# Performance work log

Hardware: AMD Instinct MI355X
Metric: run time of the kernel (lower is better)

The kernel has to match this reference:

```python
import jax, jax.numpy as jnp
import numpy as np

B, T, D, H, O = 256, 256, 256, 1024, 256


def setup_inputs() -> dict:
    key = jax.random.key(0)
    ks = jax.random.split(key, 4)
    x = jax.random.normal(ks[0], (B, T, D), dtype=jnp.float32)
    # Glorot-ish scaling to keep gates/tanh out of saturation
    Wx = jax.random.normal(ks[1], (D + O, 4 * H), dtype=jnp.float32) * 0.05
    Wh = jax.random.normal(ks[2], (H, 4 * H), dtype=jnp.float32) * 0.05
    b = jnp.zeros((4 * H,), dtype=jnp.float32)
    Wd = jax.random.normal(ks[3], (H, O), dtype=jnp.float32) * 0.05
    bd = jnp.zeros((O,), dtype=jnp.float32)
    return {"x": x, "Wx": Wx, "Wh": Wh, "b": b, "Wd": Wd, "bd": bd}


def reference(x, Wx, Wh, b, Wd, bd):
    """Autoregressive LSTM cell unrolled over time with lax.scan.

    Each step: concat(input_t, prev_dense_output) -> LSTMCell (Keras gate
    order i,f,c,o) -> Dense+tanh -> output fed back next step.
    """
    Bz = x.shape[0]
    Hh = Wh.shape[0]
    Oo = Wd.shape[1]
    h0 = jnp.zeros((Bz, Hh), dtype=x.dtype)
    c0 = jnp.zeros((Bz, Hh), dtype=x.dtype)
    y0 = jnp.zeros((Bz, Oo), dtype=x.dtype)  # initial prev_output

    def step(carry, xt):
        h, c, y = carry
        combined = jnp.concatenate([xt, y], axis=-1)  # [B, D+O]
        z = combined @ Wx + h @ Wh + b                # [B, 4H]
        i, f, g, o = jnp.split(z, 4, axis=-1)
        i = jax.nn.sigmoid(i)
        f = jax.nn.sigmoid(f)
        g = jnp.tanh(g)
        o = jax.nn.sigmoid(o)
        c_new = f * c + i * g
        h_new = o * jnp.tanh(c_new)
        y_new = jnp.tanh(h_new @ Wd + bd)             # Dense(tanh)
        return (h_new, c_new, y_new), y_new

    xs = jnp.swapaxes(x, 0, 1)  # [T, B, D]
    _, ys = jax.lax.scan(step, (h0, c0, y0), xs)
    return jnp.swapaxes(ys, 0, 1)  # [B, T, O]
```

## Files before the change

kernel.cpp:

```cpp
#include <hip/hip_runtime.h>


typedef _Float16 f16x8 __attribute__((ext_vector_type(8)));
typedef _Float16 f16x4 __attribute__((ext_vector_type(4)));
typedef float f32x4 __attribute__((ext_vector_type(4)));

#define TSTEPS 256
#define HID 1024
#define OUTD 256
#define KF 1536
#define KA 1280
#define NBLK 256
#define RSLOTS 16
#define SLOTE (256 * KA)

#define RING_OFF   0ull
#define WFULLT_OFF 0ull
#define WDT_OFF    12582912ull
#define XH_OFF     13107200ull
#define CNT_OFF    46661632ull
#define WS_NEEDED  46663680ull

#define HCNT(g) ((g) * 64)
#define YCNT(g) (128 + (g) * 64)

#define LDS_SLAB_BYTES 98304
#define LDS_WDT_BYTES  32768
#define LDS_ZBUF_BYTES 16896
#define LDS_TOTAL (LDS_SLAB_BYTES + LDS_WDT_BYTES + LDS_ZBUF_BYTES)

#define AGENT  __HIP_MEMORY_SCOPE_AGENT

__device__ __forceinline__ float sigf(float x) {
    return 1.0f / (1.0f + __expf(-x));
}
__device__ __forceinline__ float tanhfast(float x) {
    return 1.0f - 2.0f / (__expf(2.0f * x) + 1.0f);
}

__device__ __forceinline__ void garrive(int* base, int j) {
    __syncthreads();
    if (threadIdx.x == 0)
        __hip_atomic_fetch_add(base + j, 1, __ATOMIC_RELAXED, AGENT);
}
__device__ __forceinline__ void gwait(int* base, int target) {
    if (threadIdx.x < 8) {
        while (__hip_atomic_load(base + threadIdx.x, __ATOMIC_RELAXED, AGENT) < target)
            __builtin_amdgcn_s_sleep(2);
    }
    __syncthreads();
}
__device__ __forceinline__ void gwait_both(int* cnts, int target) {
    if (threadIdx.x < 8) {
        while (__hip_atomic_load(cnts + HCNT(0) + threadIdx.x, __ATOMIC_RELAXED, AGENT) < target ||
               __hip_atomic_load(cnts + HCNT(1) + threadIdx.x, __ATOMIC_RELAXED, AGENT) < target)
            __builtin_amdgcn_s_sleep(2);
    }
    __syncthreads();
}

__global__ void prep_w(const float* __restrict__ Wx, const float* __restrict__ Wh,
                       const float* __restrict__ Wd,
                       _Float16* __restrict__ WfullT, _Float16* __restrict__ WdT) {
    int bid = blockIdx.x;
    if (bid < 4096) {
        int n = bid;
        for (int k = threadIdx.x; k < KF; k += 256) {
            float v;
            if (k < 256)       v = Wx[(size_t)k * 4096 + n];
            else if (k < 1280) v = Wh[(size_t)(k - 256) * 4096 + n];
            else               v = Wx[(size_t)(k - 1024) * 4096 + n];
            WfullT[(size_t)n * KF + k] = (_Float16)v;
        }
    } else {
        int o = bid - 4096;
        for (int k = threadIdx.x; k < HID; k += 256) {
            WdT[(size_t)o * HID + k] = (_Float16)Wd[(size_t)k * OUTD + o];
        }
    }
}

__global__ void prep_x(const float* __restrict__ x, _Float16* __restrict__ xh, int* cnts) {
    size_t i0 = ((size_t)blockIdx.x * 256 + threadIdx.x) * 8;
    float4 a = *(const float4*)(x + i0);
    float4 c = *(const float4*)(x + i0 + 4);
    f16x8 v;
    v[0] = (_Float16)a.x; v[1] = (_Float16)a.y; v[2] = (_Float16)a.z; v[3] = (_Float16)a.w;
    v[4] = (_Float16)c.x; v[5] = (_Float16)c.y; v[6] = (_Float16)c.z; v[7] = (_Float16)c.w;
    *(f16x8*)(xh + i0) = v;
    if (blockIdx.x == 0) cnts[threadIdx.x] = 0;
}

template<int NS, typename AL>
__device__ __forceinline__ void gemmPart(AL&& aload, const _Float16* slab, int kbB,
                                         int rl, int kg, f32x4 (&acc)[2][2]) {
    constexpr int PFD = (NS < 12) ? NS : 12;
    f16x8 pa[PFD][2];
#pragma unroll
    for (int i = 0; i < PFD; ++i) { pa[i][0] = aload(i, 0); pa[i][1] = aload(i, 1); }
    const int sw = rl & 7;
    const _Float16* bb0 = slab + (size_t)rl * 1536;
    const _Float16* bb1 = slab + (size_t)(16 + rl) * 1536;
#pragma unroll
    for (int kk = 0; kk < NS; ++kk) {
        int kblk = kbB + kk * 4 + kg;
        int idx = (kblk ^ sw) * 8;
        f16x8 b0 = *(const f16x8*)(bb0 + idx);
        f16x8 b1 = *(const f16x8*)(bb1 + idx);
        f16x8 a0 = pa[kk % PFD][0];
        f16x8 a1 = pa[kk % PFD][1];
        if (kk + PFD < NS) {
            pa[kk % PFD][0] = aload(kk + PFD, 0);
            pa[kk % PFD][1] = aload(kk + PFD, 1);
        }
        acc[0][0] = __builtin_amdgcn_mfma_f32_16x16x32_f16(a0, b0, acc[0][0], 0, 0, 0);
        acc[0][1] = __builtin_amdgcn_mfma_f32_16x16x32_f16(a0, b1, acc[0][1], 0, 0, 0);
        acc[1][0] = __builtin_amdgcn_mfma_f32_16x16x32_f16(a1, b0, acc[1][0], 0, 0, 0);
        acc[1][1] = __builtin_amdgcn_mfma_f32_16x16x32_f16(a1, b1, acc[1][1], 0, 0, 0);
    }
}

__global__ __launch_bounds__(256, 1) void lstm_persist(
        const _Float16* __restrict__ WfullT, const _Float16* __restrict__ WdT,
        const _Float16* __restrict__ xh, const float* __restrict__ b,
        const float* __restrict__ bd,
        _Float16* __restrict__ ring,
        int* cnts, float* __restrict__ out) {
    extern __shared__ char dynsm[];
    _Float16* slab = (_Float16*)dynsm;
    _Float16* wdt  = (_Float16*)(dynsm + LDS_SLAB_BYTES);
    float* zbuf = (float*)(dynsm + LDS_SLAB_BYTES + LDS_WDT_BYTES);

    const int tid = threadIdx.x, bid = blockIdx.x;
    const int w = tid >> 6, lane = tid & 63;
    const int rl = lane & 15, kg = lane >> 4;

    const int bat0 = (bid >> 7) << 7;
    const int n0 = (bid & 127) << 3;
    const int r0 = (bid >> 4) << 4;
    const int c0 = (bid & 15) << 4;
    const int gid = bid >> 7;
    const int subj = (bid >> 4) & 7;

    int* hcnt = cnts + HCNT(gid);
    int* ycnt = cnts + YCNT(gid);

    for (int i = tid; i < 32 * 192; i += 256) {
        int vcol = i / 192, kblk = i % 192;
        int n = (vcol & 3) * 1024 + n0 + (vcol >> 2);
        f16x8 v = *(const f16x8*)(WfullT + (size_t)n * KF + kblk * 8);
        *(f16x8*)(slab + ((size_t)vcol * 192 + (kblk ^ (vcol & 7))) * 8) = v;
    }
    for (int i = tid; i < 16 * 128; i += 256) {
        int wcol = i >> 7, kb = i & 127;
        f16x8 v = *(const f16x8*)(WdT + (size_t)(c0 + wcol) * HID + kb * 8);
        *(f16x8*)(wdt + ((size_t)wcol * 128 + (kb ^ (wcol & 7))) * 8) = v;
    }
    const int trow = tid >> 1;
    const int ccB = (tid & 1) * 4;
    float bb[4][4];
#pragma unroll
    for (int g = 0; g < 4; ++g)
#pragma unroll
        for (int c2 = 0; c2 < 4; ++c2)
            bb[g][c2] = b[g * 1024 + n0 + ccB + c2];
    const float bdv = bd[c0 + (tid & 15)];
    float creg[4] = {0.f, 0.f, 0.f, 0.f};

    const size_t arow = (size_t)(bat0 + w * 32 + rl);

    auto epilogue = [&](f32x4 (&A)[2][2], _Float16* slotW) {
#pragma unroll
        for (int mt = 0; mt < 2; ++mt)
#pragma unroll
            for (int nt = 0; nt < 2; ++nt)
#pragma unroll
                for (int r = 0; r < 4; ++r) {
                    int zrow = w * 32 + mt * 16 + kg * 4 + r;
                    zbuf[zrow * 33 + nt * 16 + rl] = A[mt][nt][r];
                }
        __syncthreads();
        union { f16x4 v; unsigned long long u; } hu;
#pragma unroll
        for (int c2 = 0; c2 < 4; ++c2) {
            int cc = ccB + c2;
            float zi = zbuf[trow * 33 + cc * 4 + 0];
            float zf = zbuf[trow * 33 + cc * 4 + 1];
            float zg = zbuf[trow * 33 + cc * 4 + 2];
            float zo = zbuf[trow * 33 + cc * 4 + 3];
            float iv = sigf(zi + bb[0][c2]);
            float fv = sigf(zf + bb[1][c2]);
            float gv = tanhfast(zg + bb[2][c2]);
            float ov = sigf(zo + bb[3][c2]);
            float cnew = fv * creg[c2] + iv * gv;
            creg[c2] = cnew;
            hu.v[c2] = (_Float16)(ov * tanhfast(cnew));
        }
        __hip_atomic_store(
            (unsigned long long*)(slotW + (size_t)(bat0 + trow) * KA + n0 + ccB),
            hu.u, __ATOMIC_RELAXED, AGENT);
    };

    auto phaseB = [&](int t, _Float16* slotT, const f16x8* wa) {
        const _Float16* hp = slotT + (size_t)(r0 + rl) * KA + (w << 8) + kg * 8;
        f16x8 ha[8];
#pragma unroll
        for (int it = 0; it < 8; ++it)
            ha[it] = *(const f16x8*)(hp + it * 32);
        f32x4 accB; accB[0] = 0.f; accB[1] = 0.f; accB[2] = 0.f; accB[3] = 0.f;
#pragma unroll
        for (int it = 0; it < 8; ++it)
            accB = __builtin_amdgcn_mfma_f32_16x16x32_f16(ha[it], wa[it], accB, 0, 0, 0);
        float* red = zbuf;
#pragma unroll
        for (int r = 0; r < 4; ++r)
            red[w * 256 + (kg * 4 + r) * 16 + rl] = accB[r];
        __syncthreads();
        int rr = tid >> 4, cc = tid & 15;
        float s = red[rr * 16 + cc] + red[256 + rr * 16 + cc] +
                  red[512 + rr * 16 + cc] + red[768 + rr * 16 + cc];
        float y = tanhfast(s + bdv);
        __builtin_nontemporal_store(
            y, out + (size_t)(r0 + rr) * 65536 + (size_t)t * 256 + (c0 + cc));
        union { _Float16 h; unsigned short u; } cv; cv.h = (_Float16)y;
        unsigned short* ys = (unsigned short*)(zbuf + 1024);
        ys[tid] = cv.u;
        __syncthreads();
        if (tid < 64) {
            unsigned long long yv = *(const unsigned long long*)(ys + tid * 4);
            int row = r0 + (tid >> 2), colb = c0 + (tid & 3) * 4;
            __hip_atomic_store(
                (unsigned long long*)(slotT + (size_t)row * KA + 1024 + colb),
                yv, __ATOMIC_RELAXED, AGENT);
        }
    };

    garrive(hcnt, subj);
    gwait_both(cnts, 16);

    f32x4 acc[2][2];
#pragma unroll
    for (int mt = 0; mt < 2; ++mt)
#pragma unroll
        for (int nt = 0; nt < 2; ++nt) {
            acc[mt][nt][0] = 0.f; acc[mt][nt][1] = 0.f;
            acc[mt][nt][2] = 0.f; acc[mt][nt][3] = 0.f;
        }
    {
        const _Float16* xb = xh + arow * 65536 + kg * 8;
        auto loadX = [&](int kk, int mt) -> f16x8 {
            return *(const f16x8*)(xb + (size_t)mt * 16 * 65536 + kk * 32);
        };
        gemmPart<8>(loadX, slab, 0, rl, kg, acc);
    }
    epilogue(acc, ring);
    garrive(hcnt, subj);

    for (int t = 0; t < TSTEPS; ++t) {
        if ((t & 15) == 0)
            __builtin_amdgcn_fence(__ATOMIC_ACQUIRE, "agent");

        _Float16* slotT = ring + (size_t)(t & (RSLOTS - 1)) * SLOTE;

#pragma unroll
        for (int mt = 0; mt < 2; ++mt)
#pragma unroll
            for (int nt = 0; nt < 2; ++nt) {
                acc[mt][nt][0] = 0.f; acc[mt][nt][1] = 0.f;
                acc[mt][nt][2] = 0.f; acc[mt][nt][3] = 0.f;
            }

        if (t < TSTEPS - 1) {
            const _Float16* xb = xh + arow * 65536 + (size_t)(t + 1) * 256 + kg * 8;
            auto loadX = [&](int kk, int mt) -> f16x8 {
                return *(const f16x8*)(xb + (size_t)mt * 16 * 65536 + kk * 32);
            };
            gemmPart<8>(loadX, slab, 0, rl, kg, acc);
        }

        f16x8 wa[8];
#pragma unroll
        for (int it = 0; it < 8; ++it) {
            int kb = (w << 5) + it * 4 + kg;
            wa[it] = *(const f16x8*)(wdt + ((size_t)rl * 128 + (kb ^ (rl & 7))) * 8);
        }

        gwait(hcnt, (t + 2) * 16);
        phaseB(t, slotT, wa);

        if (t < TSTEPS - 1) {
            garrive(ycnt, subj);

            {
                const _Float16* hb = slotT + arow * KA + kg * 8;
                auto loadH = [&](int kk, int mt) -> f16x8 {
                    return *(const f16x8*)(hb + (size_t)mt * 16 * KA + kk * 32);
                };
                gemmPart<32>(loadH, slab, 32, rl, kg, acc);
            }

            gwait(ycnt, (t + 1) * 16);

            {
                const _Float16* yb = slotT + arow * KA + 1024 + kg * 8;
                auto loadY = [&](int kk, int mt) -> f16x8 {
                    return *(const f16x8*)(yb + (size_t)mt * 16 * KA + kk * 32);
                };
                gemmPart<8>(loadY, slab, 160, rl, kg, acc);
            }

            epilogue(acc, ring + (size_t)((t + 1) & (RSLOTS - 1)) * SLOTE);
            garrive(hcnt, subj);
        }
    }
}

extern "C" void kernel_launch(void* const* d_in, const int* in_sizes, int n_in,
                              void* d_out, int out_size, void* d_ws, size_t ws_size,
                              hipStream_t stream) {
    const float* x  = (const float*)d_in[0];
    const float* Wx = (const float*)d_in[1];
    const float* Wh = (const float*)d_in[2];
    const float* b  = (const float*)d_in[3];
    const float* Wd = (const float*)d_in[4];
    const float* bd = (const float*)d_in[5];
    float* out = (float*)d_out;
    char* ws = (char*)d_ws;
    if (ws_size < WS_NEEDED) return;

    _Float16* WfullT = (_Float16*)(ws + WFULLT_OFF);
    _Float16* WdT    = (_Float16*)(ws + WDT_OFF);
    _Float16* xh     = (_Float16*)(ws + XH_OFF);
    _Float16* ring   = (_Float16*)(ws + RING_OFF);
    int*      cnts   = (int*)(ws + CNT_OFF);

    static int lds_set = 0;
    if (!lds_set) {
        hipFuncSetAttribute((const void*)lstm_persist,
                            hipFuncAttributeMaxDynamicSharedMemorySize, LDS_TOTAL);
        lds_set = 1;
    }

    prep_w<<<4352, 256, 0, stream>>>(Wx, Wh, Wd, WfullT, WdT);
    prep_x<<<8192, 256, 0, stream>>>(x, xh, cnts);
    lstm_persist<<<NBLK, 256, LDS_TOTAL, stream>>>(WfullT, WdT, xh, b, bd, ring, cnts, out);
}
```

Before: 4.176 ms.

## Double threads per block and give each wave half the batch rows

The persistent LSTM kernel now launches 512 threads per block, so 8 waves each compute a 16-row M tile instead of 4 waves each doing 32 rows. The aim is more waves in flight to hide global and LDS latency in the serial per-step GEMMs, and fewer live accumulator and prefetch registers per wave. The gate epilogue and the dense-output phase are guarded so only the first 256 threads or first 4 waves do that work. In exchange, every weight fragment in LDS is now read by twice as many waves per step, and block-wide barriers span more waves.

```diff
diff --git a/kernel.cpp b/kernel.cpp
--- a/kernel.cpp
+++ b/kernel.cpp
@@ -93,11 +93,11 @@
 
 template<int NS, typename AL>
 __device__ __forceinline__ void gemmPart(AL&& aload, const _Float16* slab, int kbB,
-                                         int rl, int kg, f32x4 (&acc)[2][2]) {
+                                         int rl, int kg, f32x4 (&acc)[2]) {
     constexpr int PFD = (NS < 12) ? NS : 12;
-    f16x8 pa[PFD][2];
-#pragma unroll
-    for (int i = 0; i < PFD; ++i) { pa[i][0] = aload(i, 0); pa[i][1] = aload(i, 1); }
+    f16x8 pa[PFD];
+#pragma unroll
+    for (int i = 0; i < PFD; ++i) pa[i] = aload(i);
     const int sw = rl & 7;
     const _Float16* bb0 = slab + (size_t)rl * 1536;
     const _Float16* bb1 = slab + (size_t)(16 + rl) * 1536;
@@ -107,20 +107,14 @@
         int idx = (kblk ^ sw) * 8;
         f16x8 b0 = *(const f16x8*)(bb0 + idx);
         f16x8 b1 = *(const f16x8*)(bb1 + idx);
-        f16x8 a0 = pa[kk % PFD][0];
-        f16x8 a1 = pa[kk % PFD][1];
-        if (kk + PFD < NS) {
-            pa[kk % PFD][0] = aload(kk + PFD, 0);
-            pa[kk % PFD][1] = aload(kk + PFD, 1);
-        }
-        acc[0][0] = __builtin_amdgcn_mfma_f32_16x16x32_f16(a0, b0, acc[0][0], 0, 0, 0);
-        acc[0][1] = __builtin_amdgcn_mfma_f32_16x16x32_f16(a0, b1, acc[0][1], 0, 0, 0);
-        acc[1][0] = __builtin_amdgcn_mfma_f32_16x16x32_f16(a1, b0, acc[1][0], 0, 0, 0);
-        acc[1][1] = __builtin_amdgcn_mfma_f32_16x16x32_f16(a1, b1, acc[1][1], 0, 0, 0);
-    }
-}
-
-__global__ __launch_bounds__(256, 1) void lstm_persist(
+        f16x8 a0 = pa[kk % PFD];
+        if (kk + PFD < NS) pa[kk % PFD] = aload(kk + PFD);
+        acc[0] = __builtin_amdgcn_mfma_f32_16x16x32_f16(a0, b0, acc[0], 0, 0, 0);
+        acc[1] = __builtin_amdgcn_mfma_f32_16x16x32_f16(a0, b1, acc[1], 0, 0, 0);
+    }
+}
+
+__global__ __launch_bounds__(512, 2) void lstm_persist(
         const _Float16* __restrict__ WfullT, const _Float16* __restrict__ WdT,
         const _Float16* __restrict__ xh, const float* __restrict__ b,
         const float* __restrict__ bd,
@@ -145,13 +139,13 @@
     int* hcnt = cnts + HCNT(gid);
     int* ycnt = cnts + YCNT(gid);
 
-    for (int i = tid; i < 32 * 192; i += 256) {
+    for (int i = tid; i < 32 * 192; i += 512) {
         int vcol = i / 192, kblk = i % 192;
         int n = (vcol & 3) * 1024 + n0 + (vcol >> 2);
         f16x8 v = *(const f16x8*)(WfullT + (size_t)n * KF + kblk * 8);
         *(f16x8*)(slab + ((size_t)vcol * 192 + (kblk ^ (vcol & 7))) * 8) = v;
     }
-    for (int i = tid; i < 16 * 128; i += 256) {
+    for (int i = tid; i < 16 * 128; i += 512) {
         int wcol = i >> 7, kb = i & 127;
         f16x8 v = *(const f16x8*)(WdT + (size_t)(c0 + wcol) * HID + kb * 8);
         *(f16x8*)(wdt + ((size_t)wcol * 128 + (kb ^ (wcol & 7))) * 8) = v;
@@ -163,68 +157,72 @@
     for (int g = 0; g < 4; ++g)
 #pragma unroll
         for (int c2 = 0; c2 < 4; ++c2)
-            bb[g][c2] = b[g * 1024 + n0 + ccB + c2];
+            bb[g][c2] = b[g * 1024 + n0 + ((ccB + c2) & 7)];
     const float bdv = bd[c0 + (tid & 15)];
     float creg[4] = {0.f, 0.f, 0.f, 0.f};
 
-    const size_t arow = (size_t)(bat0 + w * 32 + rl);
-
-    auto epilogue = [&](f32x4 (&A)[2][2], _Float16* slotW) {
-#pragma unroll
-        for (int mt = 0; mt < 2; ++mt)
-#pragma unroll
-            for (int nt = 0; nt < 2; ++nt)
-#pragma unroll
-                for (int r = 0; r < 4; ++r) {
-                    int zrow = w * 32 + mt * 16 + kg * 4 + r;
-                    zbuf[zrow * 33 + nt * 16 + rl] = A[mt][nt][r];
-                }
+    const size_t arow = (size_t)(bat0 + w * 16 + rl);
+
+    auto epilogue = [&](f32x4 (&A)[2], _Float16* slotW) {
+#pragma unroll
+        for (int nt = 0; nt < 2; ++nt)
+#pragma unroll
+            for (int r = 0; r < 4; ++r) {
+                int zrow = w * 16 + kg * 4 + r;
+                zbuf[zrow * 33 + nt * 16 + rl] = A[nt][r];
+            }
         __syncthreads();
-        union { f16x4 v; unsigned long long u; } hu;
-#pragma unroll
-        for (int c2 = 0; c2 < 4; ++c2) {
-            int cc = ccB + c2;
-            float zi = zbuf[trow * 33 + cc * 4 + 0];
-            float zf = zbuf[trow * 33 + cc * 4 + 1];
-            float zg = zbuf[trow * 33 + cc * 4 + 2];
-            float zo = zbuf[trow * 33 + cc * 4 + 3];
-            float iv = sigf(zi + bb[0][c2]);
-            float fv = sigf(zf + bb[1][c2]);
-            float gv = tanhfast(zg + bb[2][c2]);
-            float ov = sigf(zo + bb[3][c2]);
-            float cnew = fv * creg[c2] + iv * gv;
-            creg[c2] = cnew;
-            hu.v[c2] = (_Float16)(ov * tanhfast(cnew));
-        }
-        __hip_atomic_store(
-            (unsigned long long*)(slotW + (size_t)(bat0 + trow) * KA + n0 + ccB),
-            hu.u, __ATOMIC_RELAXED, AGENT);
+        if (tid < 256) {
+            union { f16x4 v; unsigned long long u; } hu;
+#pragma unroll
+            for (int c2 = 0; c2 < 4; ++c2) {
+                int cc = ccB + c2;
+                float zi = zbuf[trow * 33 + cc * 4 + 0];
+                float zf = zbuf[trow * 33 + cc * 4 + 1];
+                float zg = zbuf[trow * 33 + cc * 4 + 2];
+                float zo = zbuf[trow * 33 + cc * 4 + 3];
+                float iv = sigf(zi + bb[0][c2]);
+                float fv = sigf(zf + bb[1][c2]);
+                float gv = tanhfast(zg + bb[2][c2]);
+                float ov = sigf(zo + bb[3][c2]);
+                float cnew = fv * creg[c2] + iv * gv;
+                creg[c2] = cnew;
+                hu.v[c2] = (_Float16)(ov * tanhfast(cnew));
+            }
+            __hip_atomic_store(
+                (unsigned long long*)(slotW + (size_t)(bat0 + trow) * KA + n0 + ccB),
+                hu.u, __ATOMIC_RELAXED, AGENT);
+        }
     };
 
     auto phaseB = [&](int t, _Float16* slotT, const f16x8* wa) {
-        const _Float16* hp = slotT + (size_t)(r0 + rl) * KA + (w << 8) + kg * 8;
-        f16x8 ha[8];
-#pragma unroll
-        for (int it = 0; it < 8; ++it)
-            ha[it] = *(const f16x8*)(hp + it * 32);
-        f32x4 accB; accB[0] = 0.f; accB[1] = 0.f; accB[2] = 0.f; accB[3] = 0.f;
-#pragma unroll
-        for (int it = 0; it < 8; ++it)
-            accB = __builtin_amdgcn_mfma_f32_16x16x32_f16(ha[it], wa[it], accB, 0, 0, 0);
         float* red = zbuf;
-#pragma unroll
-        for (int r = 0; r < 4; ++r)
-            red[w * 256 + (kg * 4 + r) * 16 + rl] = accB[r];
+        if (w < 4) {
+            const _Float16* hp = slotT + (size_t)(r0 + rl) * KA + (w << 8) + kg * 8;
+            f16x8 ha[8];
+#pragma unroll
+            for (int it = 0; it < 8; ++it)
+                ha[it] = *(const f16x8*)(hp + it * 32);
+            f32x4 accB; accB[0] = 0.f; accB[1] = 0.f; accB[2] = 0.f; accB[3] = 0.f;
+#pragma unroll
+            for (int it = 0; it < 8; ++it)
+                accB = __builtin_amdgcn_mfma_f32_16x16x32_f16(ha[it], wa[it], accB, 0, 0, 0);
+#pragma unroll
+            for (int r = 0; r < 4; ++r)
+                red[w * 256 + (kg * 4 + r) * 16 + rl] = accB[r];
+        }
         __syncthreads();
-        int rr = tid >> 4, cc = tid & 15;
-        float s = red[rr * 16 + cc] + red[256 + rr * 16 + cc] +
-                  red[512 + rr * 16 + cc] + red[768 + rr * 16 + cc];
-        float y = tanhfast(s + bdv);
-        __builtin_nontemporal_store(
-            y, out + (size_t)(r0 + rr) * 65536 + (size_t)t * 256 + (c0 + cc));
-        union { _Float16 h; unsigned short u; } cv; cv.h = (_Float16)y;
         unsigned short* ys = (unsigned short*)(zbuf + 1024);
-        ys[tid] = cv.u;
+        if (tid < 256) {
+            int rr = tid >> 4, cc = tid & 15;
+            float s = red[rr * 16 + cc] + red[256 + rr * 16 + cc] +
+                      red[512 + rr * 16 + cc] + red[768 + rr * 16 + cc];
+            float y = tanhfast(s + bdv);
+            __builtin_nontemporal_store(
+                y, out + (size_t)(r0 + rr) * 65536 + (size_t)t * 256 + (c0 + cc));
+            union { _Float16 h; unsigned short u; } cv; cv.h = (_Float16)y;
+            ys[tid] = cv.u;
+        }
         __syncthreads();
         if (tid < 64) {
             unsigned long long yv = *(const unsigned long long*)(ys + tid * 4);
@@ -238,18 +236,13 @@
     garrive(hcnt, subj);
     gwait_both(cnts, 16);
 
-    f32x4 acc[2][2];
-#pragma unroll
-    for (int mt = 0; mt < 2; ++mt)
-#pragma unroll
-        for (int nt = 0; nt < 2; ++nt) {
-            acc[mt][nt][0] = 0.f; acc[mt][nt][1] = 0.f;
-            acc[mt][nt][2] = 0.f; acc[mt][nt][3] = 0.f;
-        }
+    f32x4 acc[2];
+    acc[0][0] = 0.f; acc[0][1] = 0.f; acc[0][2] = 0.f; acc[0][3] = 0.f;
+    acc[1][0] = 0.f; acc[1][1] = 0.f; acc[1][2] = 0.f; acc[1][3] = 0.f;
     {
         const _Float16* xb = xh + arow * 65536 + kg * 8;
-        auto loadX = [&](int kk, int mt) -> f16x8 {
-            return *(const f16x8*)(xb + (size_t)mt * 16 * 65536 + kk * 32);
+        auto loadX = [&](int kk) -> f16x8 {
+            return *(const f16x8*)(xb + kk * 32);
         };
         gemmPart<8>(loadX, slab, 0, rl, kg, acc);
     }
@@ -262,18 +255,13 @@
 
         _Float16* slotT = ring + (size_t)(t & (RSLOTS - 1)) * SLOTE;
 
-#pragma unroll
-        for (int mt = 0; mt < 2; ++mt)
-#pragma unroll
-            for (int nt = 0; nt < 2; ++nt) {
-                acc[mt][nt][0] = 0.f; acc[mt][nt][1] = 0.f;
-                acc[mt][nt][2] = 0.f; acc[mt][nt][3] = 0.f;
-            }
+        acc[0][0] = 0.f; acc[0][1] = 0.f; acc[0][2] = 0.f; acc[0][3] = 0.f;
+        acc[1][0] = 0.f; acc[1][1] = 0.f; acc[1][2] = 0.f; acc[1][3] = 0.f;
 
         if (t < TSTEPS - 1) {
             const _Float16* xb = xh + arow * 65536 + (size_t)(t + 1) * 256 + kg * 8;
-            auto loadX = [&](int kk, int mt) -> f16x8 {
-                return *(const f16x8*)(xb + (size_t)mt * 16 * 65536 + kk * 32);
+            auto loadX = [&](int kk) -> f16x8 {
+                return *(const f16x8*)(xb + kk * 32);
             };
             gemmPart<8>(loadX, slab, 0, rl, kg, acc);
         }
@@ -281,7 +269,7 @@
         f16x8 wa[8];
 #pragma unroll
         for (int it = 0; it < 8; ++it) {
-            int kb = (w << 5) + it * 4 + kg;
+            int kb = ((w & 3) << 5) + it * 4 + kg;
             wa[it] = *(const f16x8*)(wdt + ((size_t)rl * 128 + (kb ^ (rl & 7))) * 8);
         }
 
@@ -293,8 +281,8 @@
 
             {
                 const _Float16* hb = slotT + arow * KA + kg * 8;
-                auto loadH = [&](int kk, int mt) -> f16x8 {
-                    return *(const f16x8*)(hb + (size_t)mt * 16 * KA + kk * 32);
+                auto loadH = [&](int kk) -> f16x8 {
+                    return *(const f16x8*)(hb + kk * 32);
                 };
                 gemmPart<32>(loadH, slab, 32, rl, kg, acc);
             }
@@ -303,8 +291,8 @@
 
             {
                 const _Float16* yb = slotT + arow * KA + 1024 + kg * 8;
-                auto loadY = [&](int kk, int mt) -> f16x8 {
-                    return *(const f16x8*)(yb + (size_t)mt * 16 * KA + kk * 32);
+                auto loadY = [&](int kk) -> f16x8 {
+                    return *(const f16x8*)(yb + kk * 32);
                 };
                 gemmPart<8>(loadY, slab, 160, rl, kg, acc);
             }
@@ -343,5 +331,5 @@
 
     prep_w<<<4352, 256, 0, stream>>>(Wx, Wh, Wd, WfullT, WdT);
     prep_x<<<8192, 256, 0, stream>>>(x, xh, cnts);
-    lstm_persist<<<NBLK, 256, LDS_TOTAL, stream>>>(WfullT, WdT, xh, b, bd, ring, cnts, out);
-}
+    lstm_persist<<<NBLK, 512, LDS_TOTAL, stream>>>(WfullT, WdT, xh, b, bd, ring, cnts, out);
+}
```

Measured after the change: 3.930 ms. 1.06x faster.

## Split persistent block into gate and dense warp groups with LDS flag sync

Applied to the files above, without the earlier changes.

Doubles the block to 512 threads and specializes warps: waves 0-3 run the gate GEMM and LSTM epilogue, while waves 4-7 independently run the dense/tanh output phase. Block-wide __syncthreads are replaced by per-wave LDS counters with release/acquire, so the two roles can overlap across timesteps instead of serializing within one block. It adds spin-polling in LDS and more register and LDS pressure from the doubled thread count. Correctness now rests on a hand-built intra-block protocol.

```diff
diff --git a/kernel.cpp b/kernel.cpp
--- a/kernel.cpp
+++ b/kernel.cpp
@@ -24,12 +24,22 @@
 #define HCNT(g) ((g) * 64)
 #define YCNT(g) (128 + (g) * 64)
 
-#define LDS_SLAB_BYTES 98304
-#define LDS_WDT_BYTES  32768
-#define LDS_ZBUF_BYTES 16896
-#define LDS_TOTAL (LDS_SLAB_BYTES + LDS_WDT_BYTES + LDS_ZBUF_BYTES)
-
-#define AGENT  __HIP_MEMORY_SCOPE_AGENT
+#define LDS_SLAB 98304
+#define LDS_WDT  32768
+#define LDS_ZBUF 16896
+#define LDS_RED  4096
+#define LDS_YS   512
+#define LDS_SYNC 64
+#define LDS_TOTAL (LDS_SLAB + LDS_WDT + LDS_ZBUF + LDS_RED + LDS_YS + LDS_SYNC)
+
+#define AGENT __HIP_MEMORY_SCOPE_AGENT
+#define WG    __HIP_MEMORY_SCOPE_WORKGROUP
+
+#define SY_ZS 0
+#define SY_HS 1
+#define SY_P1 2
+#define SY_P2 3
+#define SY_YA 4
 
 __device__ __forceinline__ float sigf(float x) {
     return 1.0f / (1.0f + __expf(-x));
@@ -38,25 +48,22 @@
     return 1.0f - 2.0f / (__expf(2.0f * x) + 1.0f);
 }
 
-__device__ __forceinline__ void garrive(int* base, int j) {
-    __syncthreads();
-    if (threadIdx.x == 0)
-        __hip_atomic_fetch_add(base + j, 1, __ATOMIC_RELAXED, AGENT);
-}
-__device__ __forceinline__ void gwait(int* base, int target) {
-    if (threadIdx.x < 8) {
-        while (__hip_atomic_load(base + threadIdx.x, __ATOMIC_RELAXED, AGENT) < target)
+__device__ __forceinline__ void vm0() {
+    asm volatile("s_waitcnt vmcnt(0)" ::: "memory");
+}
+__device__ __forceinline__ void ds_inc(int* c) {
+    if ((threadIdx.x & 63) == 0)
+        __hip_atomic_fetch_add(c, 1, __ATOMIC_RELEASE, WG);
+}
+__device__ __forceinline__ void ds_pollw(int* c, int target) {
+    if ((threadIdx.x & 63) == 0)
+        while (__hip_atomic_load(c, __ATOMIC_ACQUIRE, WG) < target) {}
+}
+__device__ __forceinline__ void gwaitw(const int* base, int target) {
+    int l = threadIdx.x & 63;
+    if (l < 8)
+        while (__hip_atomic_load(base + l, __ATOMIC_RELAXED, AGENT) < target)
             __builtin_amdgcn_s_sleep(2);
-    }
-    __syncthreads();
-}
-__device__ __forceinline__ void gwait_both(int* cnts, int target) {
-    if (threadIdx.x < 8) {
-        while (__hip_atomic_load(cnts + HCNT(0) + threadIdx.x, __ATOMIC_RELAXED, AGENT) < target ||
-               __hip_atomic_load(cnts + HCNT(1) + threadIdx.x, __ATOMIC_RELAXED, AGENT) < target)
-            __builtin_amdgcn_s_sleep(2);
-    }
-    __syncthreads();
 }
 
 __global__ void prep_w(const float* __restrict__ Wx, const float* __restrict__ Wh,
@@ -120,7 +127,7 @@
     }
 }
 
-__global__ __launch_bounds__(256, 1) void lstm_persist(
+__global__ __launch_bounds__(512, 2) void lstm_persist(
         const _Float16* __restrict__ WfullT, const _Float16* __restrict__ WdT,
         const _Float16* __restrict__ xh, const float* __restrict__ b,
         const float* __restrict__ bd,
@@ -128,8 +135,11 @@
         int* cnts, float* __restrict__ out) {
     extern __shared__ char dynsm[];
     _Float16* slab = (_Float16*)dynsm;
-    _Float16* wdt  = (_Float16*)(dynsm + LDS_SLAB_BYTES);
-    float* zbuf = (float*)(dynsm + LDS_SLAB_BYTES + LDS_WDT_BYTES);
+    _Float16* wdt  = (_Float16*)(dynsm + LDS_SLAB);
+    float* zbuf = (float*)(dynsm + LDS_SLAB + LDS_WDT);
+    float* red  = (float*)(dynsm + LDS_SLAB + LDS_WDT + LDS_ZBUF);
+    unsigned short* ys = (unsigned short*)(dynsm + LDS_SLAB + LDS_WDT + LDS_ZBUF + LDS_RED);
+    int* sy = (int*)(dynsm + LDS_SLAB + LDS_WDT + LDS_ZBUF + LDS_RED + LDS_YS);
 
     const int tid = threadIdx.x, bid = blockIdx.x;
     const int w = tid >> 6, lane = tid & 63;
@@ -145,123 +155,89 @@
     int* hcnt = cnts + HCNT(gid);
     int* ycnt = cnts + YCNT(gid);
 
-    for (int i = tid; i < 32 * 192; i += 256) {
+    for (int i = tid; i < 32 * 192; i += 512) {
         int vcol = i / 192, kblk = i % 192;
         int n = (vcol & 3) * 1024 + n0 + (vcol >> 2);
         f16x8 v = *(const f16x8*)(WfullT + (size_t)n * KF + kblk * 8);
         *(f16x8*)(slab + ((size_t)vcol * 192 + (kblk ^ (vcol & 7))) * 8) = v;
     }
-    for (int i = tid; i < 16 * 128; i += 256) {
+    for (int i = tid; i < 16 * 128; i += 512) {
         int wcol = i >> 7, kb = i & 127;
         f16x8 v = *(const f16x8*)(WdT + (size_t)(c0 + wcol) * HID + kb * 8);
         *(f16x8*)(wdt + ((size_t)wcol * 128 + (kb ^ (wcol & 7))) * 8) = v;
     }
+    if (tid < 16) sy[tid] = 0;
+
     const int trow = tid >> 1;
     const int ccB = (tid & 1) * 4;
     float bb[4][4];
-#pragma unroll
-    for (int g = 0; g < 4; ++g)
-#pragma unroll
-        for (int c2 = 0; c2 < 4; ++c2)
-            bb[g][c2] = b[g * 1024 + n0 + ccB + c2];
+    if (w < 4) {
+#pragma unroll
+        for (int g = 0; g < 4; ++g)
+#pragma unroll
+            for (int c2 = 0; c2 < 4; ++c2)
+                bb[g][c2] = b[g * 1024 + n0 + ccB + c2];
+    }
     const float bdv = bd[c0 + (tid & 15)];
     float creg[4] = {0.f, 0.f, 0.f, 0.f};
 
-    const size_t arow = (size_t)(bat0 + w * 32 + rl);
-
-    auto epilogue = [&](f32x4 (&A)[2][2], _Float16* slotW) {
-#pragma unroll
-        for (int mt = 0; mt < 2; ++mt)
-#pragma unroll
-            for (int nt = 0; nt < 2; ++nt)
-#pragma unroll
-                for (int r = 0; r < 4; ++r) {
-                    int zrow = w * 32 + mt * 16 + kg * 4 + r;
-                    zbuf[zrow * 33 + nt * 16 + rl] = A[mt][nt][r];
-                }
-        __syncthreads();
-        union { f16x4 v; unsigned long long u; } hu;
-#pragma unroll
-        for (int c2 = 0; c2 < 4; ++c2) {
-            int cc = ccB + c2;
-            float zi = zbuf[trow * 33 + cc * 4 + 0];
-            float zf = zbuf[trow * 33 + cc * 4 + 1];
-            float zg = zbuf[trow * 33 + cc * 4 + 2];
-            float zo = zbuf[trow * 33 + cc * 4 + 3];
-            float iv = sigf(zi + bb[0][c2]);
-            float fv = sigf(zf + bb[1][c2]);
-            float gv = tanhfast(zg + bb[2][c2]);
-            float ov = sigf(zo + bb[3][c2]);
-            float cnew = fv * creg[c2] + iv * gv;
-            creg[c2] = cnew;
-            hu.v[c2] = (_Float16)(ov * tanhfast(cnew));
-        }
-        __hip_atomic_store(
-            (unsigned long long*)(slotW + (size_t)(bat0 + trow) * KA + n0 + ccB),
-            hu.u, __ATOMIC_RELAXED, AGENT);
-    };
-
-    auto phaseB = [&](int t, _Float16* slotT, const f16x8* wa) {
-        const _Float16* hp = slotT + (size_t)(r0 + rl) * KA + (w << 8) + kg * 8;
-        f16x8 ha[8];
-#pragma unroll
-        for (int it = 0; it < 8; ++it)
-            ha[it] = *(const f16x8*)(hp + it * 32);
-        f32x4 accB; accB[0] = 0.f; accB[1] = 0.f; accB[2] = 0.f; accB[3] = 0.f;
-#pragma unroll
-        for (int it = 0; it < 8; ++it)
-            accB = __builtin_amdgcn_mfma_f32_16x16x32_f16(ha[it], wa[it], accB, 0, 0, 0);
-        float* red = zbuf;
-#pragma unroll
-        for (int r = 0; r < 4; ++r)
-            red[w * 256 + (kg * 4 + r) * 16 + rl] = accB[r];
-        __syncthreads();
-        int rr = tid >> 4, cc = tid & 15;
-        float s = red[rr * 16 + cc] + red[256 + rr * 16 + cc] +
-                  red[512 + rr * 16 + cc] + red[768 + rr * 16 + cc];
-        float y = tanhfast(s + bdv);
-        __builtin_nontemporal_store(
-            y, out + (size_t)(r0 + rr) * 65536 + (size_t)t * 256 + (c0 + cc));
-        union { _Float16 h; unsigned short u; } cv; cv.h = (_Float16)y;
-        unsigned short* ys = (unsigned short*)(zbuf + 1024);
-        ys[tid] = cv.u;
-        __syncthreads();
-        if (tid < 64) {
-            unsigned long long yv = *(const unsigned long long*)(ys + tid * 4);
-            int row = r0 + (tid >> 2), colb = c0 + (tid & 3) * 4;
+    __syncthreads();
+    if (tid == 0)
+        __hip_atomic_fetch_add(hcnt + subj, 1, __ATOMIC_RELAXED, AGENT);
+    if (tid < 8) {
+        while (__hip_atomic_load(cnts + HCNT(0) + tid, __ATOMIC_RELAXED, AGENT) < 16 ||
+               __hip_atomic_load(cnts + HCNT(1) + tid, __ATOMIC_RELAXED, AGENT) < 16)
+            __builtin_amdgcn_s_sleep(2);
+    }
+    __syncthreads();
+
+    if (w < 4) {
+        const size_t arow = (size_t)(bat0 + w * 32 + rl);
+        int zsT = 0, hsT = 0;
+
+        auto epilogue = [&](f32x4 (&A)[2][2], _Float16* slotW, int hEpochTarget) {
+#pragma unroll
+            for (int mt = 0; mt < 2; ++mt)
+#pragma unroll
+                for (int nt = 0; nt < 2; ++nt)
+#pragma unroll
+                    for (int r = 0; r < 4; ++r) {
+                        int zrow = w * 32 + mt * 16 + kg * 4 + r;
+                        zbuf[zrow * 33 + nt * 16 + rl] = A[mt][nt][r];
+                    }
+            zsT += 4;
+            ds_inc(sy + SY_ZS);
+            ds_pollw(sy + SY_ZS, zsT);
+            union { f16x4 v; unsigned long long u; } hu;
+#pragma unroll
+            for (int c2 = 0; c2 < 4; ++c2) {
+                int cc = ccB + c2;
+                float zi = zbuf[trow * 33 + cc * 4 + 0];
+                float zf = zbuf[trow * 33 + cc * 4 + 1];
+                float zg = zbuf[trow * 33 + cc * 4 + 2];
+                float zo = zbuf[trow * 33 + cc * 4 + 3];
+                float iv = sigf(zi + bb[0][c2]);
+                float fv = sigf(zf + bb[1][c2]);
+                float gv = tanhfast(zg + bb[2][c2]);
+                float ov = sigf(zo + bb[3][c2]);
+                float cnew = fv * creg[c2] + iv * gv;
+                creg[c2] = cnew;
+                hu.v[c2] = (_Float16)(ov * tanhfast(cnew));
+            }
             __hip_atomic_store(
-                (unsigned long long*)(slotT + (size_t)row * KA + 1024 + colb),
-                yv, __ATOMIC_RELAXED, AGENT);
-        }
-    };
-
-    garrive(hcnt, subj);
-    gwait_both(cnts, 16);
-
-    f32x4 acc[2][2];
-#pragma unroll
-    for (int mt = 0; mt < 2; ++mt)
-#pragma unroll
-        for (int nt = 0; nt < 2; ++nt) {
-            acc[mt][nt][0] = 0.f; acc[mt][nt][1] = 0.f;
-            acc[mt][nt][2] = 0.f; acc[mt][nt][3] = 0.f;
-        }
-    {
-        const _Float16* xb = xh + arow * 65536 + kg * 8;
-        auto loadX = [&](int kk, int mt) -> f16x8 {
-            return *(const f16x8*)(xb + (size_t)mt * 16 * 65536 + kk * 32);
+                (unsigned long long*)(slotW + (size_t)(bat0 + trow) * KA + n0 + ccB),
+                hu.u, __ATOMIC_RELAXED, AGENT);
+            vm0();
+            hsT += 4;
+            ds_inc(sy + SY_HS);
+            if (tid == 0) {
+                while (__hip_atomic_load(sy + SY_HS, __ATOMIC_ACQUIRE, WG) < hsT) {}
+                __hip_atomic_fetch_add(hcnt + subj, 1, __ATOMIC_RELAXED, AGENT);
+            }
+            (void)hEpochTarget;
         };
-        gemmPart<8>(loadX, slab, 0, rl, kg, acc);
-    }
-    epilogue(acc, ring);
-    garrive(hcnt, subj);
-
-    for (int t = 0; t < TSTEPS; ++t) {
-        if ((t & 15) == 0)
-            __builtin_amdgcn_fence(__ATOMIC_ACQUIRE, "agent");
-
-        _Float16* slotT = ring + (size_t)(t & (RSLOTS - 1)) * SLOTE;
-
+
+        f32x4 acc[2][2];
 #pragma unroll
         for (int mt = 0; mt < 2; ++mt)
 #pragma unroll
@@ -269,27 +245,39 @@
                 acc[mt][nt][0] = 0.f; acc[mt][nt][1] = 0.f;
                 acc[mt][nt][2] = 0.f; acc[mt][nt][3] = 0.f;
             }
-
-        if (t < TSTEPS - 1) {
-            const _Float16* xb = xh + arow * 65536 + (size_t)(t + 1) * 256 + kg * 8;
+        {
+            const _Float16* xb = xh + arow * 65536 + kg * 8;
             auto loadX = [&](int kk, int mt) -> f16x8 {
                 return *(const f16x8*)(xb + (size_t)mt * 16 * 65536 + kk * 32);
             };
             gemmPart<8>(loadX, slab, 0, rl, kg, acc);
         }
-
-        f16x8 wa[8];
-#pragma unroll
-        for (int it = 0; it < 8; ++it) {
-            int kb = (w << 5) + it * 4 + kg;
-            wa[it] = *(const f16x8*)(wdt + ((size_t)rl * 128 + (kb ^ (rl & 7))) * 8);
-        }
-
-        gwait(hcnt, (t + 2) * 16);
-        phaseB(t, slotT, wa);
-
-        if (t < TSTEPS - 1) {
-            garrive(ycnt, subj);
+        epilogue(acc, ring, 2);
+
+        for (int tt = 0; tt < TSTEPS - 1; ++tt) {
+            if ((tt & 15) == 0)
+                __builtin_amdgcn_fence(__ATOMIC_ACQUIRE, "agent");
+
+            const _Float16* slotT = ring + (size_t)(tt & (RSLOTS - 1)) * SLOTE;
+            _Float16* slotW = ring + (size_t)((tt + 1) & (RSLOTS - 1)) * SLOTE;
+
+#pragma unroll
+            for (int mt = 0; mt < 2; ++mt)
+#pragma unroll
+                for (int nt = 0; nt < 2; ++nt) {
+                    acc[mt][nt][0] = 0.f; acc[mt][nt][1] = 0.f;
+                    acc[mt][nt][2] = 0.f; acc[mt][nt][3] = 0.f;
+                }
+
+            {
+                const _Float16* xb = xh + arow * 65536 + (size_t)(tt + 1) * 256 + kg * 8;
+                auto loadX = [&](int kk, int mt) -> f16x8 {
+                    return *(const f16x8*)(xb + (size_t)mt * 16 * 65536 + kk * 32);
+                };
+                gemmPart<8>(loadX, slab, 0, rl, kg, acc);
+            }
+
+            gwaitw(hcnt, (tt + 2) * 16);
 
             {
                 const _Float16* hb = slotT + arow * KA + kg * 8;
@@ -299,7 +287,7 @@
                 gemmPart<32>(loadH, slab, 32, rl, kg, acc);
             }
 
-            gwait(ycnt, (t + 1) * 16);
+            gwaitw(ycnt, (tt + 1) * 16);
 
             {
                 const _Float16* yb = slotT + arow * KA + 1024 + kg * 8;
@@ -309,8 +297,74 @@
                 gemmPart<8>(loadY, slab, 160, rl, kg, acc);
             }
 
-            epilogue(acc, ring + (size_t)((t + 1) & (RSLOTS - 1)) * SLOTE);
-            garrive(hcnt, subj);
+            epilogue(acc, slotW, tt + 3);
+        }
+    } else {
+        const int w2 = w - 4;
+        const int tid2 = tid - 256;
+        int p1T = 0, p2T = 0, yaT = 0;
+
+        for (int t = 0; t < TSTEPS; ++t) {
+            if ((t & 15) == 0)
+                __builtin_amdgcn_fence(__ATOMIC_ACQUIRE, "agent");
+
+            _Float16* slotT = ring + (size_t)(t & (RSLOTS - 1)) * SLOTE;
+
+            f16x8 wa[8];
+#pragma unroll
+            for (int it = 0; it < 8; ++it) {
+                int kb = (w2 << 5) + it * 4 + kg;
+                wa[it] = *(const f16x8*)(wdt + ((size_t)rl * 128 + (kb ^ (rl & 7))) * 8);
+            }
+
+            gwaitw(hcnt, (t + 2) * 16);
+
+            {
+                const _Float16* hp = slotT + (size_t)(r0 + rl) * KA + (w2 << 8) + kg * 8;
+                f16x8 ha[8];
+#pragma unroll
+                for (int it = 0; it < 8; ++it)
+                    ha[it] = *(const f16x8*)(hp + it * 32);
+                f32x4 accB; accB[0] = 0.f; accB[1] = 0.f; accB[2] = 0.f; accB[3] = 0.f;
+#pragma unroll
+                for (int it = 0; it < 8; ++it)
+                    accB = __builtin_amdgcn_mfma_f32_16x16x32_f16(ha[it], wa[it], accB, 0, 0, 0);
+#pragma unroll
+                for (int r = 0; r < 4; ++r)
+                    red[w2 * 256 + (kg * 4 + r) * 16 + rl] = accB[r];
+            }
+            p1T += 4;
+            ds_inc(sy + SY_P1);
+            ds_pollw(sy + SY_P1, p1T);
+
+            {
+                int rr = tid2 >> 4, cc = tid2 & 15;
+                float s = red[rr * 16 + cc] + red[256 + rr * 16 + cc] +
+                          red[512 + rr * 16 + cc] + red[768 + rr * 16 + cc];
+                float y = tanhfast(s + bdv);
+                __builtin_nontemporal_store(
+                    y, out + (size_t)(r0 + rr) * 65536 + (size_t)t * 256 + (c0 + cc));
+                union { _Float16 h; unsigned short u; } cv; cv.h = (_Float16)y;
+                ys[tid2] = cv.u;
+            }
+            p2T += 4;
+            ds_inc(sy + SY_P2);
+            ds_pollw(sy + SY_P2, p2T);
+
+            if (tid2 < 64) {
+                unsigned long long yv = *(const unsigned long long*)(ys + tid2 * 4);
+                int row = r0 + (tid2 >> 2), colb = c0 + (tid2 & 3) * 4;
+                __hip_atomic_store(
+                    (unsigned long long*)(slotT + (size_t)row * KA + 1024 + colb),
+                    yv, __ATOMIC_RELAXED, AGENT);
+            }
+            vm0();
+            yaT += 4;
+            ds_inc(sy + SY_YA);
+            if (tid2 == 0) {
+                while (__hip_atomic_load(sy + SY_YA, __ATOMIC_ACQUIRE, WG) < yaT) {}
+                __hip_atomic_fetch_add(ycnt + subj, 1, __ATOMIC_RELAXED, AGENT);
+            }
         }
     }
 }
@@ -343,5 +397,5 @@
 
     prep_w<<<4352, 256, 0, stream>>>(Wx, Wh, Wd, WfullT, WdT);
     prep_x<<<8192, 256, 0, stream>>>(x, xh, cnts);
-    lstm_persist<<<NBLK, 256, LDS_TOTAL, stream>>>(WfullT, WdT, xh, b, bd, ring, cnts, out);
-}
+    lstm_persist<<<NBLK, 512, LDS_TOTAL, stream>>>(WfullT, WdT, xh, b, bd, ring, cnts, out);
+}
```

After: 6.591 ms. +57.8%, slower.
